# Kernel tuning notes

Hardware: AMD Instinct MI355X
Metric: run time of the kernel (lower is better)

The kernel has to match this reference:

```python
import jax, jax.numpy as jnp
import numpy as np

A, I = 16, 16           # n_agents, n_items
D = A * I               # flattened bid dim
ROUNDS = 40             # sinkhorn_rounds
EPS = 0.1               # sinkhorn_epsilon
B = 32768               # batch size


def setup_inputs() -> dict:
    key = jax.random.key(0)
    ks = jax.random.split(key, 20)

    def lin(k, din, dout):
        k1, k2 = jax.random.split(k)
        s = 1.0 / np.sqrt(din)
        W = jax.random.uniform(k1, (din, dout), minval=-s, maxval=s, dtype=jnp.float32)
        b = jax.random.uniform(k2, (dout,), minval=-s, maxval=s, dtype=jnp.float32)
        return W, b

    inp = {"bids": jax.random.uniform(ks[0], (B, A, I), dtype=jnp.float32)}
    dims_a = [(D, 128), (128, 128), (128, 128), (128, D)]
    dims_p = [(D, 128), (128, 128), (128, 128), (128, A)]
    for i, (din, dout) in enumerate(dims_a):
        W, b = lin(ks[1 + i], din, dout)
        inp[f"aw{i}"] = W
        inp[f"ab{i}"] = b
    for i, (din, dout) in enumerate(dims_p):
        W, b = lin(ks[5 + i], din, dout)
        inp[f"pw{i}"] = W
        inp[f"pb{i}"] = b
    return inp


def _log_sinkhorn(log_K, log_a, log_b):
    # log_K: [B, A+1, I+1]; log_a: [A+1]; log_b: [I+1]
    def step(K, _):
        K = K + (log_a - jax.scipy.special.logsumexp(K, axis=-1))[..., :, None]
        K = K + (log_b - jax.scipy.special.logsumexp(K, axis=-2))[..., None, :]
        return K, None
    K, _ = jax.lax.scan(step, log_K, None, length=ROUNDS)
    return jnp.exp(K)


def _forward(bids, aw0, ab0, aw1, ab1, aw2, ab2, aw3, ab3,
             pw0, pb0, pw1, pb1, pw2, pb2, pw3, pb3):
    bsz = bids.shape[0]
    X = bids.reshape(bsz, D)

    h = jnp.tanh(X @ aw0 + ab0)
    h = jnp.tanh(h @ aw1 + ab1)
    h = jnp.tanh(h @ aw2 + ab2)
    augmented = h @ aw3 + ab3                     # [B, A*I]

    # bipartite matching via log-domain Sinkhorn on padded matrix
    mat = augmented.reshape(bsz, A, I)
    padded = -jnp.pad(mat, ((0, 0), (0, 1), (0, 1)))  # [B, A+1, I+1]
    # 'unit' marginals: each agent/item has mass 1, dummies absorb the rest
    log_a = jnp.log(jnp.concatenate([jnp.ones(A, jnp.float32), jnp.full((1,), float(I), jnp.float32)]))
    log_b = jnp.log(jnp.concatenate([jnp.ones(I, jnp.float32), jnp.full((1,), float(A), jnp.float32)]))
    plan = _log_sinkhorn(-padded / EPS, log_a, log_b)
    allocs = plan[:, :A, :I]                      # drop dummy row/col

    p = jnp.tanh(X @ pw0 + pb0)
    p = jnp.tanh(p @ pw1 + pb1)
    p = jnp.tanh(p @ pw2 + pb2)
    frac = jax.nn.sigmoid(p @ pw3 + pb3)          # [B, A]
    payments = frac * (allocs * bids).sum(axis=-1)
    return allocs, payments


def reference(bids, aw0, ab0, aw1, ab1, aw2, ab2, aw3, ab3,
              pw0, pb0, pw1, pb1, pw2, pb2, pw3, pb3):
    return _forward(bids, aw0, ab0, aw1, ab1, aw2, ab2, aw3, ab3,
                    pw0, pb0, pw1, pb1, pw2, pb2, pw3, pb3)
```

## Files before the change

### kernel.cpp

```cpp
#include <hip/hip_runtime.h>

#define NB 32768

typedef _Float16 half8 __attribute__((ext_vector_type(8)));
typedef float floatx4 __attribute__((ext_vector_type(4)));
typedef float floatx2 __attribute__((ext_vector_type(2)));
typedef unsigned int uint4v __attribute__((ext_vector_type(4)));

#define MFMA16(a,b,c) __builtin_amdgcn_mfma_f32_16x16x32_f16(a,b,c,0,0,0)

__device__ __forceinline__ float rcp_f(float x){ return __builtin_amdgcn_rcpf(x); }
__device__ __forceinline__ float exp2_f(float x){ return __builtin_amdgcn_exp2f(x); }
__device__ __forceinline__ float tanh_f(float x){
  float e = exp2_f(x * 2.8853900817779268f);
  return (e - 1.0f) * rcp_f(e + 1.0f);
}
__device__ __forceinline__ float sigmoid_f(float x){
  return rcp_f(1.0f + exp2_f(-1.4426950408889634f * x));
}

__device__ __forceinline__ floatx2 pk_mul2(floatx2 a, floatx2 b){
  floatx2 d; asm("v_pk_mul_f32 %0, %1, %2" : "=v"(d) : "v"(a), "v"(b)); return d;
}
__device__ __forceinline__ floatx2 pk_fma2(floatx2 a, floatx2 b, floatx2 c){
  floatx2 d; asm("v_pk_fma_f32 %0, %1, %2, %3" : "=v"(d) : "v"(a), "v"(b), "v"(c)); return d;
}

template<int CTRL>
__device__ __forceinline__ float dpp_qp(float x){
  return __builtin_bit_cast(float, __builtin_amdgcn_update_dpp(0, __builtin_bit_cast(int,x), CTRL, 0xF, 0xF, true));
}
__device__ __forceinline__ float qadd2(float x){
  x += dpp_qp<0xB1>(x);
  x += dpp_qp<0x4E>(x);
  return x;
}
__device__ __forceinline__ float qmax2(float x){
  x = fmaxf(x, dpp_qp<0xB1>(x));
  x = fmaxf(x, dpp_qp<0x4E>(x));
  return x;
}

constexpr int O_AW0H = 0;
constexpr int O_AW1H = 32768;
constexpr int O_AW2H = 49152;
constexpr int O_AW3H = 65536;
constexpr int O_PW0H = 98304;
constexpr int O_PW1H = 131072;
constexpr int O_PW2H = 147456;
constexpr int O_PW3H = 163840;
constexpr int O_AW1L = 165888;
constexpr int O_AW2L = 182272;
constexpr int O_AW3L = 198656;

struct PrepJob { const float* src; _Float16* h; _Float16* l; int nshift; int total; };
struct PrepJobs { PrepJob j[8]; };

__global__ void prep_kernel(PrepJobs js){
  const PrepJob jb = js.j[blockIdx.y];
  const int idx = blockIdx.x*256 + threadIdx.x;
  if (idx >= jb.total) return;
  const int N = 1 << jb.nshift;
  const int n = idx & (N-1);
  const int k = idx >> jb.nshift;
  const int K = jb.total >> jb.nshift;
  float w = jb.src[idx];
  _Float16 h = (_Float16)w;
  jb.h[(long)n*K + k] = h;
  if (jb.l) jb.l[(long)n*K + k] = (_Float16)(w - (float)h);
}

__device__ __forceinline__ int aaddr(int row, int col){
  int cc = (col >> 2) ^ (row & 7);
  return row*128 + (cc<<2) + (col & 3);
}

template<bool NEED_LO>
__device__ __forceinline__ void read_frag(const unsigned int* __restrict__ act,
    int row, int ks, int q, half8& ah, half8& al)
{
  const int s = row & 7;
  const int cc0 = ks*8 + q*2;
  uint4v c0 = *(const uint4v*)(act + row*128 + (((cc0  ) ^ s)<<2));
  uint4v c1 = *(const uint4v*)(act + row*128 + (((cc0+1) ^ s)<<2));
  uint4v h;
  h.x = (c0.x & 0xffffu) | (c0.y << 16);
  h.y = (c0.z & 0xffffu) | (c0.w << 16);
  h.z = (c1.x & 0xffffu) | (c1.y << 16);
  h.w = (c1.z & 0xffffu) | (c1.w << 16);
  ah = __builtin_bit_cast(half8, h);
  if constexpr (NEED_LO){
    uint4v g;
    g.x = (c0.x >> 16) | (c0.y & 0xffff0000u);
    g.y = (c0.z >> 16) | (c0.w & 0xffff0000u);
    g.z = (c1.x >> 16) | (c1.y & 0xffff0000u);
    g.w = (c1.z >> 16) | (c1.w & 0xffff0000u);
    al = __builtin_bit_cast(half8, g);
  }
}

__device__ __forceinline__ unsigned int pack_act(float v){
  _Float16 h = (_Float16)v;
  _Float16 lo = (_Float16)(v - (float)h);
  return (unsigned int)__builtin_bit_cast(unsigned short, h)
       | ((unsigned int)__builtin_bit_cast(unsigned short, lo) << 16);
}
__device__ __forceinline__ unsigned int pack_act_hi(float v){
  return (unsigned int)__builtin_bit_cast(unsigned short, (_Float16)v);
}

template<int KS, bool LO>
__device__ __forceinline__ void load_tile(
    const _Float16* __restrict__ Wh, const _Float16* __restrict__ Wl,
    int K, int nt, int l15, int q, half8* bh, half8* bl)
{
  const _Float16* bp = Wh + (nt*16 + l15)*K + q*8;
#pragma unroll
  for (int ks=0; ks<KS; ++ks) bh[ks] = *(const half8*)(bp + ks*32);
  if constexpr (LO){
    const _Float16* blp = Wl + (nt*16 + l15)*K + q*8;
#pragma unroll
    for (int ks=0; ks<KS; ++ks) bl[ks] = *(const half8*)(blp + ks*32);
  }
}

template<int KS, int PASSES, int NT, int RING, typename EPI>
__device__ __forceinline__ void mfma_stream2(
    const half8* Ah0, const half8* Al0,
    const half8* Ah1, const half8* Al1,
    const _Float16* __restrict__ Wh, const _Float16* __restrict__ Wl,
    int K, int nt0, int l15, int q, EPI&& epi)
{
  half8 Bh[RING][KS], Bl[RING][KS];
  load_tile<KS,PASSES==3>(Wh, Wl, K, nt0, l15, q, Bh[0], Bl[0]);
  if constexpr (RING > 2){
    if constexpr (NT > 1)
      load_tile<KS,PASSES==3>(Wh, Wl, K, nt0+1, l15, q, Bh[1], Bl[1]);
  }
#pragma unroll
  for (int nt=0; nt<NT; ++nt){
    constexpr int PD = RING - 1;
    if (nt+PD < NT)
      load_tile<KS,PASSES==3>(Wh, Wl, K, nt0+nt+PD, l15, q, Bh[(nt+PD)%RING], Bl[(nt+PD)%RING]);
    floatx4 a0e=(floatx4)0.0f, a0o=(floatx4)0.0f;
    floatx4 a1e=(floatx4)0.0f, a1o=(floatx4)0.0f;
#pragma unroll
    for (int ks=0; ks<KS; ++ks){
      const half8 bh = Bh[nt%RING][ks];
      floatx4& c0 = (ks & 1) ? a0o : a0e;
      floatx4& c1 = (ks & 1) ? a1o : a1e;
      c0 = MFMA16(Ah0[ks], bh, c0);
      c1 = MFMA16(Ah1[ks], bh, c1);
      if constexpr (PASSES == 3){
        const half8 bl = Bl[nt%RING][ks];
        c0 = MFMA16(Al0[ks], bh, c0);
        c0 = MFMA16(Ah0[ks], bl, c0);
        c1 = MFMA16(Al1[ks], bh, c1);
        c1 = MFMA16(Ah1[ks], bl, c1);
      }
    }
    floatx4 acc0, acc1;
#pragma unroll
    for (int r=0; r<4; ++r){ acc0[r] = a0e[r] + a0o[r]; acc1[r] = a1e[r] + a1o[r]; }
    epi(nt0+nt, acc0, acc1);
  }
}

__global__ __launch_bounds__(128, 2) void fused_kernel(
  const float* __restrict__ X, const _Float16* __restrict__ WT,
  const float* __restrict__ ab0, const float* __restrict__ ab1,
  const float* __restrict__ ab2, const float* __restrict__ ab3,
  const float* __restrict__ pb0, const float* __restrict__ pb1,
  const float* __restrict__ pb2, const float* __restrict__ pb3,
  float* __restrict__ out)
{
  __shared__ unsigned int S[32*256 + 512];
  unsigned int* act_a = S;
  unsigned int* act_p = S + 4096;
  float* frac_l = (float*)(S + 8192);
  const int t = threadIdx.x;
  const int w = t >> 6;
  const int l = t & 63, q = l>>4, l15 = l&15;
  const int nt0 = w*4;
  const long rb = (long)blockIdx.x * 32;

  auto epi_act = [&](unsigned int* act, const float* bias, bool lo){
    return [=](int ntg, floatx4 acc0, floatx4 acc1){
      float bb = bias[ntg*16 + l15];
#pragma unroll
      for (int r=0; r<4; ++r){
        float t0 = tanh_f(acc0[r] + bb);
        act[aaddr(q*4 + r, ntg*16 + l15)] = lo ? pack_act(t0) : pack_act_hi(t0);
      }
#pragma unroll
      for (int r=0; r<4; ++r){
        float t1 = tanh_f(acc1[r] + bb);
        act[aaddr(16 + q*4 + r, ntg*16 + l15)] = lo ? pack_act(t1) : pack_act_hi(t1);
      }
    };
  };

  {
    half8 Xf0[8], Xf1[8];
#pragma unroll
    for (int mt=0; mt<2; ++mt){
      float4 xa[8], xb[8];
#pragma unroll
      for (int ks=0; ks<8; ++ks){
        const float* xp = X + (rb + mt*16 + l15)*256 + ks*32 + q*8;
        xa[ks] = *(const float4*)(xp);
        xb[ks] = *(const float4*)(xp + 4);
      }
      half8* Xf = mt ? Xf1 : Xf0;
#pragma unroll
      for (int ks=0; ks<8; ++ks){
        half8 h;
        h[0]=(_Float16)xa[ks].x; h[1]=(_Float16)xa[ks].y; h[2]=(_Float16)xa[ks].z; h[3]=(_Float16)xa[ks].w;
        h[4]=(_Float16)xb[ks].x; h[5]=(_Float16)xb[ks].y; h[6]=(_Float16)xb[ks].z; h[7]=(_Float16)xb[ks].w;
        Xf[ks] = h;
      }
    }
    mfma_stream2<8,1,4,2>(Xf0, Xf0, Xf1, Xf1, WT+O_AW0H, WT+O_AW0H, 256, nt0, l15, q,
                          epi_act(act_a, ab0, true));
    mfma_stream2<8,1,4,2>(Xf0, Xf0, Xf1, Xf1, WT+O_PW0H, WT+O_PW0H, 256, nt0, l15, q,
                          epi_act(act_p, pb0, false));
  }
  __syncthreads();

#pragma unroll 1
  for (int st=0; st<2; ++st){
    const _Float16* Wah = WT + (st ? O_AW2H : O_AW1H);
    const _Float16* Wal = WT + (st ? O_AW2L : O_AW1L);
    const _Float16* Wph = WT + (st ? O_PW2H : O_PW1H);
    const float* ba = st ? ab2 : ab1;
    const float* bp = st ? pb2 : pb1;
    half8 Aa0[4], Ala0[4], Aa1[4], Ala1[4], Ap0[4], Ap1[4], du;
#pragma unroll
    for (int ks=0; ks<4; ++ks){
      read_frag<true >(act_a, l15,      ks, q, Aa0[ks], Ala0[ks]);
      read_frag<true >(act_a, 16 + l15, ks, q, Aa1[ks], Ala1[ks]);
      read_frag<false>(act_p, l15,      ks, q, Ap0[ks], du);
      read_frag<false>(act_p, 16 + l15, ks, q, Ap1[ks], du);
    }
    __syncthreads();
    mfma_stream2<4,3,4,2>(Aa0, Ala0, Aa1, Ala1, Wah, Wal, 128, nt0, l15, q,
                          epi_act(act_a, ba, true));
    mfma_stream2<4,1,4,3>(Ap0, Ap0, Ap1, Ap1, Wph, Wph, 128, nt0, l15, q,
                          epi_act(act_p, bp, false));
    __syncthreads();
  }

  {
    half8 Aa0[4], Ala0[4], Aa1[4], Ala1[4], Ap0[4], Ap1[4], du;
#pragma unroll
    for (int ks=0; ks<4; ++ks){
      read_frag<true>(act_a, l15,      ks, q, Aa0[ks], Ala0[ks]);
      read_frag<true>(act_a, 16 + l15, ks, q, Aa1[ks], Ala1[ks]);
    }
    if (w == 0){
#pragma unroll
      for (int ks=0; ks<4; ++ks){
        read_frag<false>(act_p, l15,      ks, q, Ap0[ks], du);
        read_frag<false>(act_p, 16 + l15, ks, q, Ap1[ks], du);
      }
    }
    __syncthreads();
    if (w == 0){
      mfma_stream2<4,1,1,2>(Ap0, Ap0, Ap1, Ap1, WT+O_PW3H, WT+O_PW3H, 128, 0, l15, q,
        [&](int, floatx4 a0, floatx4 a1){
          float bb = pb3[l15];
#pragma unroll
          for (int r=0; r<4; ++r){
            frac_l[(q*4+r)*16 + l15]    = sigmoid_f(a0[r] + bb);
            frac_l[(16+q*4+r)*16 + l15] = sigmoid_f(a1[r] + bb);
          }
        });
    }
    float* augl = (float*)S;
    const int ncol0 = w*128;
    mfma_stream2<4,3,8,2>(Aa0, Ala0, Aa1, Ala1,
                          WT+O_AW3H + w*128*128, WT+O_AW3L + w*128*128,
                          128, 0, l15, q,
      [&](int nt, floatx4 a0, floatx4 a1){
        float bb = ab3[ncol0 + nt*16 + l15];
#pragma unroll
        for (int r=0; r<4; ++r){
          augl[(q*4+r)*256 + ncol0 + nt*16 + l15]    = a0[r] + bb;
          augl[(16+q*4+r)*256 + ncol0 + nt*16 + l15] = a1[r] + bb;
        }
      });
    __syncthreads();
  }

  const int c = l & 3;
  const float Ssc = 14.426950408889634f;
  const float cmask = (c == 3) ? 1.0f : 0.0f;
  const int eL = w*16 + (l >> 2);
  const long e = rb + eL;

  floatx2 Kp[4][8];
  floatx2 KPp[8];

  const float* ap = (const float*)S + eL*256 + 4*c;
#pragma unroll
  for (int k=0;k<8;++k){
    float4 va = *(const float4*)(ap + (2*k  )*16);
    float4 vb = *(const float4*)(ap + (2*k+1)*16);
    Kp[0][k] = (floatx2){va.x*Ssc, vb.x*Ssc};
    Kp[1][k] = (floatx2){va.y*Ssc, vb.y*Ssc};
    Kp[2][k] = (floatx2){va.z*Ssc, vb.z*Ssc};
    Kp[3][k] = (floatx2){va.w*Ssc, vb.w*Ssc};
  }

#pragma unroll
  for (int k=0;k<8;++k){
    float m0 = fmaxf(fmaxf(Kp[0][k].x,Kp[1][k].x), fmaxf(Kp[2][k].x,Kp[3][k].x));
    m0 = qmax2(fmaxf(m0, 0.0f));
    float m1 = fmaxf(fmaxf(Kp[0][k].y,Kp[1][k].y), fmaxf(Kp[2][k].y,Kp[3][k].y));
    m1 = qmax2(fmaxf(m1, 0.0f));
    Kp[0][k] = (floatx2){exp2_f(Kp[0][k].x-m0), exp2_f(Kp[0][k].y-m1)};
    Kp[1][k] = (floatx2){exp2_f(Kp[1][k].x-m0), exp2_f(Kp[1][k].y-m1)};
    Kp[2][k] = (floatx2){exp2_f(Kp[2][k].x-m0), exp2_f(Kp[2][k].y-m1)};
    Kp[3][k] = (floatx2){exp2_f(Kp[3][k].x-m0), exp2_f(Kp[3][k].y-m1)};
    KPp[k]   = (floatx2){cmask*exp2_f(-m0), cmask*exp2_f(-m1)};
  }

  float vj0=1.f, vj1=1.f, vj2=1.f, vj3=1.f;
  float v16 = cmask;
  floatx2 u2[8];
  float u16;

  for (int r=0;r<40;++r){
    floatx2 b0=(floatx2){vj0,vj0}, b1=(floatx2){vj1,vj1};
    floatx2 b2=(floatx2){vj2,vj2}, b3=(floatx2){vj3,vj3};
    floatx2 b16=(floatx2){v16,v16};
#pragma unroll
    for (int k=0;k<8;++k){
      floatx2 pp = pk_mul2(Kp[0][k], b0);
      pp = pk_fma2(Kp[1][k], b1, pp);
      pp = pk_fma2(Kp[2][k], b2, pp);
      pp = pk_fma2(Kp[3][k], b3, pp);
      pp = pk_fma2(KPp[k], b16, pp);
      float px = qadd2(pp.x);
      float py = qadd2(pp.y);
      u2[k] = (floatx2){rcp_f(px), rcp_f(py)};
    }
    {
      float p16 = (vj0+vj1) + (vj2+vj3) + cmask*v16;
      p16 = qadd2(p16);
      u16 = 16.0f * rcp_f(p16);
    }
    floatx2 t0p = pk_mul2(Kp[0][0], u2[0]);
    floatx2 t1p = pk_mul2(Kp[1][0], u2[0]);
    floatx2 t2p = pk_mul2(Kp[2][0], u2[0]);
    floatx2 t3p = pk_mul2(Kp[3][0], u2[0]);
    floatx2 tPp = pk_mul2(KPp[0],   u2[0]);
#pragma unroll
    for (int k=1;k<8;++k){
      t0p = pk_fma2(Kp[0][k], u2[k], t0p);
      t1p = pk_fma2(Kp[1][k], u2[k], t1p);
      t2p = pk_fma2(Kp[2][k], u2[k], t2p);
      t3p = pk_fma2(Kp[3][k], u2[k], t3p);
      tPp = pk_fma2(KPp[k],   u2[k], tPp);
    }
    float t0 = t0p.x + t0p.y + u16;
    float t1 = t1p.x + t1p.y + u16;
    float t2 = t2p.x + t2p.y + u16;
    float t3 = t3p.x + t3p.y + u16;
    float t16 = tPp.x + tPp.y + cmask*u16;
    vj0 = rcp_f(t0); vj1 = rcp_f(t1); vj2 = rcp_f(t2); vj3 = rcp_f(t3);
    v16 = cmask * 16.0f * rcp_f(t16 + 1e-30f + (1.0f - cmask));
  }

  float* op = out + e*256 + 4*c;
  const float* bpx = X + e*256 + 4*c;
  float pv0=0.f, pv1=0.f, pv2=0.f, pv3=0.f;
#pragma unroll
  for (int k=0;k<8;++k){
#pragma unroll
    for (int h=0;h<2;++h){
      const int i = 2*k + h;
      const float uu = h ? u2[k].y : u2[k].x;
      const float K0 = h ? Kp[0][k].y : Kp[0][k].x;
      const float K1 = h ? Kp[1][k].y : Kp[1][k].x;
      const float K2 = h ? Kp[2][k].y : Kp[2][k].x;
      const float K3 = h ? Kp[3][k].y : Kp[3][k].x;
      float4 wv;
      wv.x = uu*K0*vj0;
      wv.y = uu*K1*vj1;
      wv.z = uu*K2*vj2;
      wv.w = uu*K3*vj3;
      *(float4*)(op + i*16) = wv;
      float4 bb = *(const float4*)(bpx + i*16);
      float s = wv.x*bb.x + wv.y*bb.y + wv.z*bb.z + wv.w*bb.w;
      s = qadd2(s);
      if ((i>>2) == c){
        const int rr = i & 3;
        if      (rr==0) pv0 = s;
        else if (rr==1) pv1 = s;
        else if (rr==2) pv2 = s;
        else            pv3 = s;
      }
    }
  }
  const float4 fr = *(const float4*)(frac_l + eL*16 + 4*c);
  float4 pvv;
  pvv.x = pv0*fr.x; pvv.y = pv1*fr.y; pvv.z = pv2*fr.z; pvv.w = pv3*fr.w;
  *(float4*)(out + (size_t)NB*256 + e*16 + 4*c) = pvv;
}

extern "C" void kernel_launch(void* const* d_in, const int* in_sizes, int n_in,
                              void* d_out, int out_size, void* d_ws, size_t ws_size,
                              hipStream_t stream)
{
  const float* bids = (const float*)d_in[0];
  const float* aw0 = (const float*)d_in[1];  const float* ab0 = (const float*)d_in[2];
  const float* aw1 = (const float*)d_in[3];  const float* ab1 = (const float*)d_in[4];
  const float* aw2 = (const float*)d_in[5];  const float* ab2 = (const float*)d_in[6];
  const float* aw3 = (const float*)d_in[7];  const float* ab3 = (const float*)d_in[8];
  const float* pw0 = (const float*)d_in[9];  const float* pb0 = (const float*)d_in[10];
  const float* pw1 = (const float*)d_in[11]; const float* pb1 = (const float*)d_in[12];
  const float* pw2 = (const float*)d_in[13]; const float* pb2 = (const float*)d_in[14];
  const float* pw3 = (const float*)d_in[15]; const float* pb3 = (const float*)d_in[16];

  _Float16* WT = (_Float16*)d_ws;

  PrepJobs js;
  js.j[0] = { aw0, WT+O_AW0H, nullptr,    7, 32768 };
  js.j[1] = { aw1, WT+O_AW1H, WT+O_AW1L,  7, 16384 };
  js.j[2] = { aw2, WT+O_AW2H, WT+O_AW2L,  7, 16384 };
  js.j[3] = { aw3, WT+O_AW3H, WT+O_AW3L,  8, 32768 };
  js.j[4] = { pw0, WT+O_PW0H, nullptr,    7, 32768 };
  js.j[5] = { pw1, WT+O_PW1H, nullptr,    7, 16384 };
  js.j[6] = { pw2, WT+O_PW2H, nullptr,    7, 16384 };
  js.j[7] = { pw3, WT+O_PW3H, nullptr,    4, 2048  };

  prep_kernel<<<dim3(128,8), 256, 0, stream>>>(js);
  fused_kernel<<<dim3(NB/32), 128, 0, stream>>>(bids, WT, ab0,ab1,ab2,ab3,
                                                pb0,pb1,pb2,pb3, (float*)d_out);
}
```

Baseline: 198.7 us.

## Split activations into padded hi/lo fp16 planes and fuse alloc/payment hidden stages

The packed hi|lo 32-bit activation layout with XOR swizzle is replaced by separate fp16 hi and lo planes using a 17-half8 row stride for padding. MFMA fragments now come from single 16-byte LDS reads instead of two reads plus bit-unpacking. The two middle hidden layers are restructured into a stage_dual routine that interleaves the alloc and payment MFMA streams per output tile with double-buffered weight loads. The aim is fewer ALU instructions and more overlap between the two networks, at the cost of more sub-word LDS stores and possibly higher register pressure.

```diff
diff --git a/kernel.cpp b/kernel.cpp
--- a/kernel.cpp
+++ b/kernel.cpp
@@ -5,7 +5,6 @@
 typedef _Float16 half8 __attribute__((ext_vector_type(8)));
 typedef float floatx4 __attribute__((ext_vector_type(4)));
 typedef float floatx2 __attribute__((ext_vector_type(2)));
-typedef unsigned int uint4v __attribute__((ext_vector_type(4)));
 
 #define MFMA16(a,b,c) __builtin_amdgcn_mfma_f32_16x16x32_f16(a,b,c,0,0,0)
 
@@ -70,43 +69,18 @@
   if (jb.l) jb.l[(long)n*K + k] = (_Float16)(w - (float)h);
 }
 
-__device__ __forceinline__ int aaddr(int row, int col){
-  int cc = (col >> 2) ^ (row & 7);
-  return row*128 + (cc<<2) + (col & 3);
-}
-
-template<bool NEED_LO>
-__device__ __forceinline__ void read_frag(const unsigned int* __restrict__ act,
-    int row, int ks, int q, half8& ah, half8& al)
-{
-  const int s = row & 7;
-  const int cc0 = ks*8 + q*2;
-  uint4v c0 = *(const uint4v*)(act + row*128 + (((cc0  ) ^ s)<<2));
-  uint4v c1 = *(const uint4v*)(act + row*128 + (((cc0+1) ^ s)<<2));
-  uint4v h;
-  h.x = (c0.x & 0xffffu) | (c0.y << 16);
-  h.y = (c0.z & 0xffffu) | (c0.w << 16);
-  h.z = (c1.x & 0xffffu) | (c1.y << 16);
-  h.w = (c1.z & 0xffffu) | (c1.w << 16);
-  ah = __builtin_bit_cast(half8, h);
-  if constexpr (NEED_LO){
-    uint4v g;
-    g.x = (c0.x >> 16) | (c0.y & 0xffff0000u);
-    g.y = (c0.z >> 16) | (c0.w & 0xffff0000u);
-    g.z = (c1.x >> 16) | (c1.y & 0xffff0000u);
-    g.w = (c1.z >> 16) | (c1.w & 0xffff0000u);
-    al = __builtin_bit_cast(half8, g);
-  }
-}
-
-__device__ __forceinline__ unsigned int pack_act(float v){
+__device__ __forceinline__ half8 ld_frag(const _Float16* __restrict__ a, int row, int ks, int q){
+  return *(const half8*)(a + (row*17 + ks*4 + q)*8);
+}
+__device__ __forceinline__ void st_hl(_Float16* __restrict__ ah, _Float16* __restrict__ al,
+                                      int row, int col, float v){
+  const int o = (row*17 + (col>>3))*8 + (col&7);
   _Float16 h = (_Float16)v;
-  _Float16 lo = (_Float16)(v - (float)h);
-  return (unsigned int)__builtin_bit_cast(unsigned short, h)
-       | ((unsigned int)__builtin_bit_cast(unsigned short, lo) << 16);
-}
-__device__ __forceinline__ unsigned int pack_act_hi(float v){
-  return (unsigned int)__builtin_bit_cast(unsigned short, (_Float16)v);
+  ah[o] = h;
+  al[o] = (_Float16)(v - (float)h);
+}
+__device__ __forceinline__ void st_h(_Float16* __restrict__ ah, int row, int col, float v){
+  ah[(row*17 + (col>>3))*8 + (col&7)] = (_Float16)v;
 }
 
 template<int KS, bool LO>
@@ -166,6 +140,68 @@
   }
 }
 
+__device__ __forceinline__ void stage_dual(
+    _Float16* __restrict__ aAh, _Float16* __restrict__ aAl, _Float16* __restrict__ aPh,
+    const _Float16* __restrict__ Wah, const _Float16* __restrict__ Wal,
+    const float* __restrict__ ba,
+    const _Float16* __restrict__ Wph, const float* __restrict__ bpp,
+    int nt0, int l15, int q)
+{
+  half8 Fa0h[4], Fa0l[4], Fa1h[4], Fa1l[4], Fp0[4], Fp1[4];
+#pragma unroll
+  for (int ks=0; ks<4; ++ks){
+    Fa0h[ks] = ld_frag(aAh, l15,      ks, q);
+    Fa0l[ks] = ld_frag(aAl, l15,      ks, q);
+    Fa1h[ks] = ld_frag(aAh, 16 + l15, ks, q);
+    Fa1l[ks] = ld_frag(aAl, 16 + l15, ks, q);
+    Fp0[ks]  = ld_frag(aPh, l15,      ks, q);
+    Fp1[ks]  = ld_frag(aPh, 16 + l15, ks, q);
+  }
+  __syncthreads();
+
+  half8 Bah[2][4], Bal[2][4], Bph[2][4];
+  load_tile<4,true >(Wah, Wal, 128, nt0, l15, q, Bah[0], Bal[0]);
+  load_tile<4,false>(Wph, Wph, 128, nt0, l15, q, Bph[0], Bph[0]);
+#pragma unroll
+  for (int nt=0; nt<4; ++nt){
+    if (nt+1 < 4){
+      load_tile<4,true >(Wah, Wal, 128, nt0+nt+1, l15, q, Bah[(nt+1)&1], Bal[(nt+1)&1]);
+      load_tile<4,false>(Wph, Wph, 128, nt0+nt+1, l15, q, Bph[(nt+1)&1], Bph[(nt+1)&1]);
+    }
+    floatx4 a0e=(floatx4)0.0f, a0o=(floatx4)0.0f;
+    floatx4 a1e=(floatx4)0.0f, a1o=(floatx4)0.0f;
+    floatx4 p0 =(floatx4)0.0f, p1 =(floatx4)0.0f;
+#pragma unroll
+    for (int ks=0; ks<4; ++ks){
+      const half8 bh = Bah[nt&1][ks], bl = Bal[nt&1][ks];
+      floatx4& c0 = (ks & 1) ? a0o : a0e;
+      floatx4& c1 = (ks & 1) ? a1o : a1e;
+      c0 = MFMA16(Fa0h[ks], bh, c0);
+      c1 = MFMA16(Fa1h[ks], bh, c1);
+      c0 = MFMA16(Fa0l[ks], bh, c0);
+      c0 = MFMA16(Fa0h[ks], bl, c0);
+      c1 = MFMA16(Fa1l[ks], bh, c1);
+      c1 = MFMA16(Fa1h[ks], bl, c1);
+    }
+#pragma unroll
+    for (int ks=0; ks<4; ++ks){
+      p0 = MFMA16(Fp0[ks], Bph[nt&1][ks], p0);
+      p1 = MFMA16(Fp1[ks], Bph[nt&1][ks], p1);
+    }
+    const int ntg = nt0 + nt;
+    const float bba = ba [ntg*16 + l15];
+    const float bbp = bpp[ntg*16 + l15];
+#pragma unroll
+    for (int r=0; r<4; ++r){
+      st_hl(aAh, aAl,      q*4 + r, ntg*16 + l15, tanh_f(a0e[r] + a0o[r] + bba));
+      st_hl(aAh, aAl, 16 + q*4 + r, ntg*16 + l15, tanh_f(a1e[r] + a1o[r] + bba));
+      st_h (aPh,           q*4 + r, ntg*16 + l15, tanh_f(p0[r] + bbp));
+      st_h (aPh,      16 + q*4 + r, ntg*16 + l15, tanh_f(p1[r] + bbp));
+    }
+  }
+  __syncthreads();
+}
+
 __global__ __launch_bounds__(128, 2) void fused_kernel(
   const float* __restrict__ X, const _Float16* __restrict__ WT,
   const float* __restrict__ ab0, const float* __restrict__ ab1,
@@ -174,9 +210,10 @@
   const float* __restrict__ pb2, const float* __restrict__ pb3,
   float* __restrict__ out)
 {
-  __shared__ unsigned int S[32*256 + 512];
-  unsigned int* act_a = S;
-  unsigned int* act_p = S + 4096;
+  __shared__ unsigned int S[8704];
+  _Float16* act_a_h = (_Float16*)S;
+  _Float16* act_a_l = (_Float16*)S + 4352;
+  _Float16* act_p_h = (_Float16*)S + 8704;
   float* frac_l = (float*)(S + 8192);
   const int t = threadIdx.x;
   const int w = t >> 6;
@@ -184,22 +221,6 @@
   const int nt0 = w*4;
   const long rb = (long)blockIdx.x * 32;
 
-  auto epi_act = [&](unsigned int* act, const float* bias, bool lo){
-    return [=](int ntg, floatx4 acc0, floatx4 acc1){
-      float bb = bias[ntg*16 + l15];
-#pragma unroll
-      for (int r=0; r<4; ++r){
-        float t0 = tanh_f(acc0[r] + bb);
-        act[aaddr(q*4 + r, ntg*16 + l15)] = lo ? pack_act(t0) : pack_act_hi(t0);
-      }
-#pragma unroll
-      for (int r=0; r<4; ++r){
-        float t1 = tanh_f(acc1[r] + bb);
-        act[aaddr(16 + q*4 + r, ntg*16 + l15)] = lo ? pack_act(t1) : pack_act_hi(t1);
-      }
-    };
-  };
-
   {
     half8 Xf0[8], Xf1[8];
 #pragma unroll
@@ -221,52 +242,48 @@
       }
     }
     mfma_stream2<8,1,4,2>(Xf0, Xf0, Xf1, Xf1, WT+O_AW0H, WT+O_AW0H, 256, nt0, l15, q,
-                          epi_act(act_a, ab0, true));
+      [&](int ntg, floatx4 a0, floatx4 a1){
+        float bb = ab0[ntg*16 + l15];
+#pragma unroll
+        for (int r=0; r<4; ++r){
+          st_hl(act_a_h, act_a_l,      q*4 + r, ntg*16 + l15, tanh_f(a0[r] + bb));
+          st_hl(act_a_h, act_a_l, 16 + q*4 + r, ntg*16 + l15, tanh_f(a1[r] + bb));
+        }
+      });
     mfma_stream2<8,1,4,2>(Xf0, Xf0, Xf1, Xf1, WT+O_PW0H, WT+O_PW0H, 256, nt0, l15, q,
-                          epi_act(act_p, pb0, false));
+      [&](int ntg, floatx4 a0, floatx4 a1){
+        float bb = pb0[ntg*16 + l15];
+#pragma unroll
+        for (int r=0; r<4; ++r){
+          st_h(act_p_h,      q*4 + r, ntg*16 + l15, tanh_f(a0[r] + bb));
+          st_h(act_p_h, 16 + q*4 + r, ntg*16 + l15, tanh_f(a1[r] + bb));
+        }
+      });
   }
   __syncthreads();
 
-#pragma unroll 1
-  for (int st=0; st<2; ++st){
-    const _Float16* Wah = WT + (st ? O_AW2H : O_AW1H);
-    const _Float16* Wal = WT + (st ? O_AW2L : O_AW1L);
-    const _Float16* Wph = WT + (st ? O_PW2H : O_PW1H);
-    const float* ba = st ? ab2 : ab1;
-    const float* bp = st ? pb2 : pb1;
-    half8 Aa0[4], Ala0[4], Aa1[4], Ala1[4], Ap0[4], Ap1[4], du;
+  stage_dual(act_a_h, act_a_l, act_p_h, WT+O_AW1H, WT+O_AW1L, ab1, WT+O_PW1H, pb1, nt0, l15, q);
+  stage_dual(act_a_h, act_a_l, act_p_h, WT+O_AW2H, WT+O_AW2L, ab2, WT+O_PW2H, pb2, nt0, l15, q);
+
+  {
+    half8 Fa0h[4], Fa0l[4], Fa1h[4], Fa1l[4], Fp0[4], Fp1[4];
 #pragma unroll
     for (int ks=0; ks<4; ++ks){
-      read_frag<true >(act_a, l15,      ks, q, Aa0[ks], Ala0[ks]);
-      read_frag<true >(act_a, 16 + l15, ks, q, Aa1[ks], Ala1[ks]);
-      read_frag<false>(act_p, l15,      ks, q, Ap0[ks], du);
-      read_frag<false>(act_p, 16 + l15, ks, q, Ap1[ks], du);
-    }
-    __syncthreads();
-    mfma_stream2<4,3,4,2>(Aa0, Ala0, Aa1, Ala1, Wah, Wal, 128, nt0, l15, q,
-                          epi_act(act_a, ba, true));
-    mfma_stream2<4,1,4,3>(Ap0, Ap0, Ap1, Ap1, Wph, Wph, 128, nt0, l15, q,
-                          epi_act(act_p, bp, false));
-    __syncthreads();
-  }
-
-  {
-    half8 Aa0[4], Ala0[4], Aa1[4], Ala1[4], Ap0[4], Ap1[4], du;
-#pragma unroll
-    for (int ks=0; ks<4; ++ks){
-      read_frag<true>(act_a, l15,      ks, q, Aa0[ks], Ala0[ks]);
-      read_frag<true>(act_a, 16 + l15, ks, q, Aa1[ks], Ala1[ks]);
+      Fa0h[ks] = ld_frag(act_a_h, l15,      ks, q);
+      Fa0l[ks] = ld_frag(act_a_l, l15,      ks, q);
+      Fa1h[ks] = ld_frag(act_a_h, 16 + l15, ks, q);
+      Fa1l[ks] = ld_frag(act_a_l, 16 + l15, ks, q);
     }
     if (w == 0){
 #pragma unroll
       for (int ks=0; ks<4; ++ks){
-        read_frag<false>(act_p, l15,      ks, q, Ap0[ks], du);
-        read_frag<false>(act_p, 16 + l15, ks, q, Ap1[ks], du);
+        Fp0[ks] = ld_frag(act_p_h, l15,      ks, q);
+        Fp1[ks] = ld_frag(act_p_h, 16 + l15, ks, q);
       }
     }
     __syncthreads();
     if (w == 0){
-      mfma_stream2<4,1,1,2>(Ap0, Ap0, Ap1, Ap1, WT+O_PW3H, WT+O_PW3H, 128, 0, l15, q,
+      mfma_stream2<4,1,1,2>(Fp0, Fp0, Fp1, Fp1, WT+O_PW3H, WT+O_PW3H, 128, 0, l15, q,
         [&](int, floatx4 a0, floatx4 a1){
           float bb = pb3[l15];
 #pragma unroll
@@ -278,7 +295,7 @@
     }
     float* augl = (float*)S;
     const int ncol0 = w*128;
-    mfma_stream2<4,3,8,2>(Aa0, Ala0, Aa1, Ala1,
+    mfma_stream2<4,3,8,2>(Fa0h, Fa0l, Fa1h, Fa1l,
                           WT+O_AW3H + w*128*128, WT+O_AW3L + w*128*128,
                           128, 0, l15, q,
       [&](int nt, floatx4 a0, floatx4 a1){
```

New measurement: 194.6 us. -2.1%, faster.
